# Kernel optimization log

Measured on AMD Instinct MI355X. Metric: run time of the kernel, lower is better.

The kernel has to match this reference:

```python
import jax, jax.numpy as jnp
import numpy as np

B, N, F_IN, H, MH, STEPS = 8192, 9, 15, 128, 256, 4
E_PER = 16
MASK_IDX = jnp.arange(8)  # mask = [True]*8 + [False]


def setup_inputs() -> dict:
    key = jax.random.key(0)
    ks = jax.random.split(key, 24)
    s = 0.05
    inp = {
        "obs": jax.random.normal(ks[0], (B, 135), jnp.float32),
        "edges": jax.random.randint(ks[1], (B, 2, E_PER), 0, N, jnp.int32),
        "enc_W": jax.random.normal(ks[2], (F_IN, H), jnp.float32) * s,
        "enc_b": jax.random.normal(ks[3], (H,), jnp.float32) * s,
        "msg_W1": jax.random.normal(ks[4], (STEPS, 2 * H, MH), jnp.float32) * s,
        "msg_b1": jax.random.normal(ks[5], (STEPS, MH), jnp.float32) * s,
        "msg_W2": jax.random.normal(ks[6], (STEPS, MH, MH), jnp.float32) * s,
        "msg_b2": jax.random.normal(ks[7], (STEPS, MH), jnp.float32) * s,
        "msg_W3": jax.random.normal(ks[8], (STEPS, MH, H), jnp.float32) * s,
        "msg_b3": jax.random.normal(ks[9], (STEPS, H), jnp.float32) * s,
        "gru_Wi": jax.random.normal(ks[10], (STEPS, H, 3 * H), jnp.float32) * s,
        "gru_Wh": jax.random.normal(ks[11], (STEPS, H, 3 * H), jnp.float32) * s,
        "gru_bi": jax.random.normal(ks[12], (STEPS, 3 * H), jnp.float32) * s,
        "gru_bh": jax.random.normal(ks[13], (STEPS, 3 * H), jnp.float32) * s,
        "dec_W1": jax.random.normal(ks[14], (H, MH), jnp.float32) * s,
        "dec_b1": jax.random.normal(ks[15], (MH,), jnp.float32) * s,
        "dec_W2": jax.random.normal(ks[16], (MH, MH), jnp.float32) * s,
        "dec_b2": jax.random.normal(ks[17], (MH,), jnp.float32) * s,
        "dec_W3": jax.random.normal(ks[18], (MH, 1), jnp.float32) * s,
        "dec_b3": jax.random.normal(ks[19], (1,), jnp.float32) * s,
    }
    return inp


def reference(obs, edges, enc_W, enc_b, msg_W1, msg_b1, msg_W2, msg_b2,
              msg_W3, msg_b3, gru_Wi, gru_Wh, gru_bi, gru_bh,
              dec_W1, dec_b1, dec_W2, dec_b2, dec_W3, dec_b3):
    BN = B * N
    x = obs.reshape(BN, F_IN)                       # [B*N, 15]
    x = jnp.tanh(x @ enc_W + enc_b)                 # encoder -> [B*N, H]

    # flatten per-graph edges into a global edge list, then add self-loops
    offsets = (jnp.arange(B, dtype=jnp.int32) * N)[:, None, None]
    eg = edges + offsets                            # [B, 2, 16]
    loops = jnp.arange(BN, dtype=jnp.int32)
    src = jnp.concatenate([eg[:, 0, :].reshape(-1), loops])  # x_j (source)
    dst = jnp.concatenate([eg[:, 1, :].reshape(-1), loops])  # x_i (target)
    deg = jax.ops.segment_sum(jnp.ones_like(dst, dtype=x.dtype), dst,
                              num_segments=BN)      # >=1 due to self-loops

    for s in range(STEPS):
        m = jnp.concatenate([x[dst], x[src]], axis=-1)       # [E, 2H]
        m = jnp.tanh(m @ msg_W1[s] + msg_b1[s])
        m = jnp.tanh(m @ msg_W2[s] + msg_b2[s])
        m = m @ msg_W3[s] + msg_b3[s]                        # [E, H]
        aggr = jax.ops.segment_sum(m, dst, num_segments=BN) / deg[:, None]
        # GRUCell(input=aggr, hidden=x), PyTorch gate order (r, z, n)
        gi = aggr @ gru_Wi[s] + gru_bi[s]
        gh = x @ gru_Wh[s] + gru_bh[s]
        ir, iz, inn = jnp.split(gi, 3, axis=-1)
        hr, hz, hn = jnp.split(gh, 3, axis=-1)
        r = jax.nn.sigmoid(ir + hr)
        z = jax.nn.sigmoid(iz + hz)
        n = jnp.tanh(inn + r * hn)
        x = (1.0 - z) * n + z * x

    d = jnp.tanh(x @ dec_W1 + dec_b1)
    d = jnp.tanh(d @ dec_W2 + dec_b2)
    d = d @ dec_W3 + dec_b3                                  # [B*N, 1]
    out = d.reshape(B, N)
    return out[:, MASK_IDX]                                  # [B, 8]
```

## Files before the change

### kernel.cpp

```cpp
#include <hip/hip_runtime.h>
#include <hip/hip_bf16.h>
#include <math.h>

#define BGR   8192
#define NND   9
#define BN    73728
#define NE    131072
#define ETOT  204800
#define H     128
#define MH    256
#define FIN   15

typedef __bf16 bf16_t;
typedef bf16_t bf16x8 __attribute__((ext_vector_type(8)));
typedef float  f32x4  __attribute__((ext_vector_type(4)));

__device__ __forceinline__ unsigned short f2bf(float f) {
    unsigned int u = __float_as_uint(f);
    u += 0x7fff + ((u >> 16) & 1);
    return (unsigned short)(u >> 16);
}
__device__ __forceinline__ unsigned int pkbf(float a, float b) {
    union { __hip_bfloat162 h; unsigned int u; } un;
    un.h = __float22bfloat162_rn(make_float2(a, b));
    return un.u;
}
__device__ __forceinline__ bf16x8 as_frag(int4 v) {
    union { int4 i; bf16x8 f; } u; u.i = v; return u.f;
}
__device__ __forceinline__ float fast_tanh(float v) {
    float e = __expf(2.0f * v);
    return 1.0f - __fdividef(2.0f, e + 1.0f);
}
__device__ __forceinline__ int sw_off(int m, int k) {
    return m * 256 + ((((k >> 3) ^ (m & 7)) << 3) | (k & 7));
}

__global__ void deg_kernel(const int* __restrict__ edges, float* __restrict__ inv_deg) {
    int g = blockIdx.x * 256 + threadIdx.x;
    if (g >= BGR) return;
    int cnt[NND];
#pragma unroll
    for (int n = 0; n < NND; ++n) cnt[n] = 1;
    for (int j = 0; j < 16; ++j) {
        int d = edges[g * 32 + 16 + j];
#pragma unroll
        for (int n = 0; n < NND; ++n) cnt[n] += (d == n) ? 1 : 0;
    }
#pragma unroll
    for (int n = 0; n < NND; ++n) inv_deg[g * NND + n] = 1.0f / (float)cnt[n];
}

__global__ void enc_kernel(const float* __restrict__ obs, const float* __restrict__ W,
                           const float* __restrict__ b, float* __restrict__ x) {
    int tid = blockIdx.x * 256 + threadIdx.x;
    int i = tid >> 7, h = tid & 127;
    float acc = b[h];
#pragma unroll
    for (int k = 0; k < FIN; ++k) acc += obs[i * FIN + k] * W[k * H + h];
    x[i * H + h] = tanhf(acc);
}

__global__ void wt_kernel(const float* __restrict__ W1, const float* __restrict__ W2,
                          const float* __restrict__ W3, const float* __restrict__ Wi,
                          const float* __restrict__ Wh, const float* __restrict__ dW1,
                          const float* __restrict__ dW2, unsigned short* __restrict__ out) {
    int idx = blockIdx.x * 256 + threadIdx.x;
    float v;
    if (idx < 262144) {
        int s = idx >> 16, r = idx & 65535, n = r >> 8, k = r & 255;
        v = W1[(s << 16) + (k << 8) + n];
    } else if (idx < 524288) {
        int i2 = idx - 262144;
        int s = i2 >> 16, r = i2 & 65535, n = r >> 8, k = r & 255;
        v = W2[(s << 16) + (k << 8) + n];
    } else if (idx < 655360) {
        int i3 = idx - 524288;
        int s = i3 >> 15, r = i3 & 32767, n = r >> 8, k = r & 255;
        v = W3[(s << 15) + (k << 7) + n];
    } else if (idx < 1179648) {
        int i4 = idx - 655360;
        int s = i4 >> 17, rr = i4 & 131071;
        int p = rr >> 8, k = rr & 255;
        int w = p >> 6, rem = p & 63;
        int gate = rem >> 4, c = rem & 15;
        int h = w * 16 + c;
        const int sb = s * 49152;
        if (gate == 0)      v = (k < 128) ? Wi[sb + k * 384 + h]       : Wh[sb + (k - 128) * 384 + h];
        else if (gate == 1) v = (k < 128) ? Wi[sb + k * 384 + 128 + h] : Wh[sb + (k - 128) * 384 + 128 + h];
        else if (gate == 2) v = (k < 128) ? Wi[sb + k * 384 + 256 + h] : 0.f;
        else                v = (k < 128) ? 0.f                        : Wh[sb + (k - 128) * 384 + 256 + h];
    } else if (idx < 1212416) {
        int i5 = idx - 1179648;
        int n = i5 >> 7, k = i5 & 127;
        v = dW1[k * 256 + n];
    } else {
        int i6 = idx - 1212416;
        int n = i6 >> 8, k = i6 & 255;
        v = dW2[k * 256 + n];
    }
    out[idx] = f2bf(v);
}

__global__ __launch_bounds__(512, 4) void msg_mfma(
        const float* __restrict__ x, const int* __restrict__ edges,
        const unsigned short* __restrict__ W1T, const float* __restrict__ b1,
        const unsigned short* __restrict__ W2T, const float* __restrict__ b2,
        const unsigned short* __restrict__ W3T,
        float* __restrict__ aggr) {
    __shared__ unsigned short buf[64 * 256];
    __shared__ int sdst[64];
    const int t  = threadIdx.x;
    const int e0 = blockIdx.x * 64;
    const int wv = t >> 6;
    const int ln = t & 63;
    const int lrow = ln & 15;
    const int lq   = ln >> 4;

    if (t < 64) {
        const int eg = e0 + t;
        sdst[t] = (eg < NE) ? ((eg >> 4) * NND + edges[(eg >> 4) * 32 + 16 + (eg & 15)])
                            : (eg - NE);
    }
    {
        const int row  = t >> 2;
        const int q    = t & 3;
        const int e    = row & 63;
        const int side = row >> 6;
        const int eg   = e0 + e;
        int node;
        if (eg < NE) {
            int g = eg >> 4, j = eg & 15;
            node = g * NND + (side ? edges[g * 32 + j] : edges[g * 32 + 16 + j]);
        } else {
            node = eg - NE;
        }
        const float* xs = x + (size_t)node * H + q * 32;
        const int kbase = side * 128 + q * 32;
#pragma unroll
        for (int i = 0; i < 8; ++i) {
            float4 v = *(const float4*)(xs + i * 4);
            uint2 o;
            o.x = pkbf(v.x, v.y); o.y = pkbf(v.z, v.w);
            *(uint2*)(buf + sw_off(e, kbase + i * 4)) = o;
        }
    }
    __syncthreads();

    const f32x4 zero = {0.f, 0.f, 0.f, 0.f};
    const int nbase = wv * 32;

    {
        f32x4 acc[4][2];
#pragma unroll
        for (int i = 0; i < 4; ++i)
#pragma unroll
            for (int j = 0; j < 2; ++j) acc[i][j] = zero;
        for (int kq = 0; kq < 8; ++kq) {
            const int ko = kq * 32 + lq * 8;
            bf16x8 af[4], bfr[2];
#pragma unroll
            for (int tm = 0; tm < 4; ++tm)
                af[tm] = as_frag(*(const int4*)(buf + sw_off(tm * 16 + lrow, ko)));
#pragma unroll
            for (int tn = 0; tn < 2; ++tn)
                bfr[tn] = as_frag(*(const int4*)(W1T + (size_t)(nbase + tn * 16 + lrow) * 256 + ko));
#pragma unroll
            for (int tm = 0; tm < 4; ++tm)
#pragma unroll
                for (int tn = 0; tn < 2; ++tn)
                    acc[tm][tn] = __builtin_amdgcn_mfma_f32_16x16x32_bf16(af[tm], bfr[tn], acc[tm][tn], 0, 0, 0);
        }
        __syncthreads();
#pragma unroll
        for (int tn = 0; tn < 2; ++tn) {
            const int n = nbase + tn * 16 + lrow;
            const float bias = b1[n];
#pragma unroll
            for (int tm = 0; tm < 4; ++tm)
#pragma unroll
                for (int r = 0; r < 4; ++r) {
                    const int m = tm * 16 + lq * 4 + r;
                    buf[sw_off(m, n)] = f2bf(fast_tanh(acc[tm][tn][r] + bias));
                }
        }
    }
    __syncthreads();

    {
        f32x4 acc[4][2];
#pragma unroll
        for (int i = 0; i < 4; ++i)
#pragma unroll
            for (int j = 0; j < 2; ++j) acc[i][j] = zero;
        for (int kq = 0; kq < 8; ++kq) {
            const int ko = kq * 32 + lq * 8;
            bf16x8 af[4], bfr[2];
#pragma unroll
            for (int tm = 0; tm < 4; ++tm)
                af[tm] = as_frag(*(const int4*)(buf + sw_off(tm * 16 + lrow, ko)));
#pragma unroll
            for (int tn = 0; tn < 2; ++tn)
                bfr[tn] = as_frag(*(const int4*)(W2T + (size_t)(nbase + tn * 16 + lrow) * 256 + ko));
#pragma unroll
            for (int tm = 0; tm < 4; ++tm)
#pragma unroll
                for (int tn = 0; tn < 2; ++tn)
                    acc[tm][tn] = __builtin_amdgcn_mfma_f32_16x16x32_bf16(af[tm], bfr[tn], acc[tm][tn], 0, 0, 0);
        }
        __syncthreads();
#pragma unroll
        for (int tn = 0; tn < 2; ++tn) {
            const int n = nbase + tn * 16 + lrow;
            const float bias = b2[n];
#pragma unroll
            for (int tm = 0; tm < 4; ++tm)
#pragma unroll
                for (int r = 0; r < 4; ++r) {
                    const int m = tm * 16 + lq * 4 + r;
                    buf[sw_off(m, n)] = f2bf(fast_tanh(acc[tm][tn][r] + bias));
                }
        }
    }
    __syncthreads();

    {
        const int n = wv * 16 + lrow;
        f32x4 acc3[4];
#pragma unroll
        for (int i = 0; i < 4; ++i) acc3[i] = zero;
        for (int kq = 0; kq < 8; ++kq) {
            const int ko = kq * 32 + lq * 8;
            bf16x8 af[4];
#pragma unroll
            for (int tm = 0; tm < 4; ++tm)
                af[tm] = as_frag(*(const int4*)(buf + sw_off(tm * 16 + lrow, ko)));
            const bf16x8 bfr = as_frag(*(const int4*)(W3T + (size_t)n * 256 + ko));
#pragma unroll
            for (int tm = 0; tm < 4; ++tm)
                acc3[tm] = __builtin_amdgcn_mfma_f32_16x16x32_bf16(af[tm], bfr, acc3[tm], 0, 0, 0);
        }
#pragma unroll
        for (int tm = 0; tm < 4; ++tm)
#pragma unroll
            for (int r = 0; r < 4; ++r) {
                const int m = tm * 16 + lq * 4 + r;
                atomicAdd(aggr + (size_t)sdst[m] * H + n, acc3[tm][r]);
            }
    }
}

__global__ __launch_bounds__(512, 4) void gru_mfma(
        float* __restrict__ x, float* __restrict__ aggr, const float* __restrict__ inv_deg,
        const unsigned short* __restrict__ WG, const float* __restrict__ b3m,
        const float* __restrict__ bi, const float* __restrict__ bh) {
    __shared__ unsigned short bufA[64 * 256];
    const int t = threadIdx.x;
    const int n0 = blockIdx.x * 64;
    const int wv = t >> 6, ln = t & 63, lrow = ln & 15, lq = ln >> 4;

    {
        const int m = t >> 3;
        const int q = t & 7;
        const int k0 = q * 32;
        const int node = n0 + m;
        if (q < 4) {
            const float scale = inv_deg[node];
            const float* src = aggr + (size_t)node * H + k0;
#pragma unroll
            for (int i = 0; i < 8; ++i) {
                float4 v = *(const float4*)(src + i * 4);
                const float4 bb = *(const float4*)(b3m + k0 + i * 4);
                v.x = v.x * scale + bb.x; v.y = v.y * scale + bb.y;
                v.z = v.z * scale + bb.z; v.w = v.w * scale + bb.w;
                uint2 o; o.x = pkbf(v.x, v.y); o.y = pkbf(v.z, v.w);
                *(uint2*)(bufA + sw_off(m, k0 + i * 4)) = o;
            }
        } else {
            const float* src = x + (size_t)node * H + (k0 - 128);
#pragma unroll
            for (int i = 0; i < 8; ++i) {
                float4 v = *(const float4*)(src + i * 4);
                uint2 o; o.x = pkbf(v.x, v.y); o.y = pkbf(v.z, v.w);
                *(uint2*)(bufA + sw_off(m, k0 + i * 4)) = o;
            }
        }
    }
    __syncthreads();

    const f32x4 zero = {0.f, 0.f, 0.f, 0.f};
    f32x4 acc[4][4];
#pragma unroll
    for (int i = 0; i < 4; ++i)
#pragma unroll
        for (int j = 0; j < 4; ++j) acc[i][j] = zero;

    for (int kq = 0; kq < 8; ++kq) {
        const int ko = kq * 32 + lq * 8;
        bf16x8 af[4], bfr[4];
#pragma unroll
        for (int tm = 0; tm < 4; ++tm)
            af[tm] = as_frag(*(const int4*)(bufA + sw_off(tm * 16 + lrow, ko)));
#pragma unroll
        for (int g = 0; g < 4; ++g)
            bfr[g] = as_frag(*(const int4*)(WG + (size_t)(wv * 64 + g * 16 + lrow) * 256 + ko));
#pragma unroll
        for (int tm = 0; tm < 4; ++tm)
#pragma unroll
            for (int g = 0; g < 4; ++g)
                acc[tm][g] = __builtin_amdgcn_mfma_f32_16x16x32_bf16(af[tm], bfr[g], acc[tm][g], 0, 0, 0);
    }

    {
        const int h = wv * 16 + lrow;
        const float b_r = bi[h] + bh[h];
        const float b_z = bi[128 + h] + bh[128 + h];
        const float b_n = bi[256 + h];
        const float b_h = bh[256 + h];
#pragma unroll
        for (int tm = 0; tm < 4; ++tm) {
#pragma unroll
            for (int r = 0; r < 4; ++r) {
                const int node = n0 + tm * 16 + lq * 4 + r;
                const float irhr = acc[tm][0][r] + b_r;
                const float izhz = acc[tm][1][r] + b_z;
                const float inn  = acc[tm][2][r] + b_n;
                const float hn   = acc[tm][3][r] + b_h;
                const float rg = 1.f / (1.f + expf(-irhr));
                const float zg = 1.f / (1.f + expf(-izhz));
                const float ng = tanhf(inn + rg * hn);
                const float xo = x[(size_t)node * H + h];
                x[(size_t)node * H + h] = (1.f - zg) * ng + zg * xo;
                aggr[(size_t)node * H + h] = 0.f;
            }
        }
    }
}

__global__ __launch_bounds__(256, 4) void dec_mfma(
        const float* __restrict__ x,
        const unsigned short* __restrict__ W1T, const float* __restrict__ b1,
        const unsigned short* __restrict__ W2T, const float* __restrict__ b2,
        const float* __restrict__ W3, const float* __restrict__ b3,
        float* __restrict__ out) {
    __shared__ unsigned short buf[64 * 256];
    const int t = threadIdx.x;
    const int id0 = blockIdx.x * 64;
    const int wv = t >> 6, ln = t & 63, lrow = ln & 15, lq = ln >> 4;
    const int nbase = wv * 64;

    {
        const int m = t >> 2, q = t & 3;
        const int id = id0 + m;
        const int node = (id >> 3) * NND + (id & 7);
        const float* src = x + (size_t)node * H + q * 32;
#pragma unroll
        for (int i = 0; i < 8; ++i) {
            float4 v = *(const float4*)(src + i * 4);
            uint2 o; o.x = pkbf(v.x, v.y); o.y = pkbf(v.z, v.w);
            *(uint2*)(buf + sw_off(m, q * 32 + i * 4)) = o;
        }
    }
    __syncthreads();

    const f32x4 zero = {0.f, 0.f, 0.f, 0.f};

    {
        f32x4 acc[4][4];
#pragma unroll
        for (int i = 0; i < 4; ++i)
#pragma unroll
            for (int j = 0; j < 4; ++j) acc[i][j] = zero;
        for (int kq = 0; kq < 4; ++kq) {
            const int ko = kq * 32 + lq * 8;
            bf16x8 af[4], bfr[4];
#pragma unroll
            for (int tm = 0; tm < 4; ++tm)
                af[tm] = as_frag(*(const int4*)(buf + sw_off(tm * 16 + lrow, ko)));
#pragma unroll
            for (int tn = 0; tn < 4; ++tn)
                bfr[tn] = as_frag(*(const int4*)(W1T + (size_t)(nbase + tn * 16 + lrow) * 128 + ko));
#pragma unroll
            for (int tm = 0; tm < 4; ++tm)
#pragma unroll
                for (int tn = 0; tn < 4; ++tn)
                    acc[tm][tn] = __builtin_amdgcn_mfma_f32_16x16x32_bf16(af[tm], bfr[tn], acc[tm][tn], 0, 0, 0);
        }
        __syncthreads();
#pragma unroll
        for (int tn = 0; tn < 4; ++tn) {
            const int n = nbase + tn * 16 + lrow;
            const float bias = b1[n];
#pragma unroll
            for (int tm = 0; tm < 4; ++tm)
#pragma unroll
                for (int r = 0; r < 4; ++r) {
                    const int m = tm * 16 + lq * 4 + r;
                    buf[sw_off(m, n)] = f2bf(fast_tanh(acc[tm][tn][r] + bias));
                }
        }
    }
    __syncthreads();

    {
        f32x4 acc[4][4];
#pragma unroll
        for (int i = 0; i < 4; ++i)
#pragma unroll
            for (int j = 0; j < 4; ++j) acc[i][j] = zero;
        for (int kq = 0; kq < 8; ++kq) {
            const int ko = kq * 32 + lq * 8;
            bf16x8 af[4], bfr[4];
#pragma unroll
            for (int tm = 0; tm < 4; ++tm)
                af[tm] = as_frag(*(const int4*)(buf + sw_off(tm * 16 + lrow, ko)));
#pragma unroll
            for (int tn = 0; tn < 4; ++tn)
                bfr[tn] = as_frag(*(const int4*)(W2T + (size_t)(nbase + tn * 16 + lrow) * 256 + ko));
#pragma unroll
            for (int tm = 0; tm < 4; ++tm)
#pragma unroll
                for (int tn = 0; tn < 4; ++tn)
                    acc[tm][tn] = __builtin_amdgcn_mfma_f32_16x16x32_bf16(af[tm], bfr[tn], acc[tm][tn], 0, 0, 0);
        }
        __syncthreads();
#pragma unroll
        for (int tn = 0; tn < 4; ++tn) {
            const int n = nbase + tn * 16 + lrow;
            const float bias = b2[n];
#pragma unroll
            for (int tm = 0; tm < 4; ++tm)
#pragma unroll
                for (int r = 0; r < 4; ++r) {
                    const int m = tm * 16 + lq * 4 + r;
                    buf[sw_off(m, n)] = f2bf(fast_tanh(acc[tm][tn][r] + bias));
                }
        }
    }
    __syncthreads();

    {
        const int m = t >> 2, p = t & 3;
        float s = 0.f;
#pragma unroll
        for (int i = 0; i < 64; ++i) {
            const int k = p * 64 + i;
            const float a = __uint_as_float((unsigned int)buf[sw_off(m, k)] << 16);
            s += a * W3[k];
        }
        s += __shfl_xor(s, 1);
        s += __shfl_xor(s, 2);
        if (p == 0) out[id0 + m] = s + b3[0];
    }
}

extern "C" void kernel_launch(void* const* d_in, const int* in_sizes, int n_in,
                              void* d_out, int out_size, void* d_ws, size_t ws_size,
                              hipStream_t stream) {
    const float* obs    = (const float*)d_in[0];
    const int*   edges  = (const int*)  d_in[1];
    const float* enc_W  = (const float*)d_in[2];
    const float* enc_b  = (const float*)d_in[3];
    const float* msg_W1 = (const float*)d_in[4];
    const float* msg_b1 = (const float*)d_in[5];
    const float* msg_W2 = (const float*)d_in[6];
    const float* msg_b2 = (const float*)d_in[7];
    const float* msg_W3 = (const float*)d_in[8];
    const float* msg_b3 = (const float*)d_in[9];
    const float* gru_Wi = (const float*)d_in[10];
    const float* gru_Wh = (const float*)d_in[11];
    const float* gru_bi = (const float*)d_in[12];
    const float* gru_bh = (const float*)d_in[13];
    const float* dec_W1 = (const float*)d_in[14];
    const float* dec_b1 = (const float*)d_in[15];
    const float* dec_W2 = (const float*)d_in[16];
    const float* dec_b2 = (const float*)d_in[17];
    const float* dec_W3 = (const float*)d_in[18];
    const float* dec_b3 = (const float*)d_in[19];

    float* x       = (float*)d_ws;
    float* aggr    = x + (size_t)BN * H;
    float* inv_deg = aggr + (size_t)BN * H;
    unsigned short* wbf = (unsigned short*)(inv_deg + BN);

    hipMemsetAsync(aggr, 0, (size_t)BN * H * sizeof(float), stream);
    deg_kernel<<<(BGR + 255) / 256, 256, 0, stream>>>(edges, inv_deg);
    wt_kernel<<<1277952 / 256, 256, 0, stream>>>(msg_W1, msg_W2, msg_W3, gru_Wi, gru_Wh,
                                                 dec_W1, dec_W2, wbf);
    enc_kernel<<<BN * H / 256, 256, 0, stream>>>(obs, enc_W, enc_b, x);

    for (int s = 0; s < 4; ++s) {
        const unsigned short* W1T = wbf + (size_t)s * 65536;
        const unsigned short* W2T = wbf + 262144 + (size_t)s * 65536;
        const unsigned short* W3T = wbf + 524288 + (size_t)s * 32768;
        const unsigned short* WGs = wbf + 655360 + (size_t)s * 131072;
        msg_mfma<<<ETOT / 64, 512, 0, stream>>>(
            x, edges,
            W1T, msg_b1 + (size_t)s * 256,
            W2T, msg_b2 + (size_t)s * 256,
            W3T,
            aggr);
        gru_mfma<<<BN / 64, 512, 0, stream>>>(
            x, aggr, inv_deg, WGs, msg_b3 + (size_t)s * 128,
            gru_bi + (size_t)s * 384, gru_bh + (size_t)s * 384);
    }

    dec_mfma<<<BGR * 8 / 64, 256, 0, stream>>>(
        x, wbf + 1179648, dec_b1, wbf + 1212416, dec_b2, dec_W3, dec_b3, (float*)d_out);
}
```

Baseline: 1.416 ms.

## Switch message MLP to 32x32x16 MFMA with double-buffered LDS

Rewrites the per-edge message MLP kernel to use 32x32x16 bf16 MFMA tiles instead of 16x16x32, with a 16-way XOR swizzle and two LDS buffers that alternate between layers. Alternating buffers removes the extra barrier that separated the last MFMA read from the activation writeback in each layer. The larger tile raises the compute done per fragment load, but the second 32 KB buffer doubles LDS use per block and may lower occupancy. The GRU and decoder kernels also get their k-loops fully unrolled and a hoisted weight pointer.

```diff
diff --git a/kernel.cpp b/kernel.cpp
--- a/kernel.cpp
+++ b/kernel.cpp
@@ -14,6 +14,7 @@
 typedef __bf16 bf16_t;
 typedef bf16_t bf16x8 __attribute__((ext_vector_type(8)));
 typedef float  f32x4  __attribute__((ext_vector_type(4)));
+typedef float  f32x16 __attribute__((ext_vector_type(16)));
 
 __device__ __forceinline__ unsigned short f2bf(float f) {
     unsigned int u = __float_as_uint(f);
@@ -31,6 +32,9 @@
 __device__ __forceinline__ float fast_tanh(float v) {
     float e = __expf(2.0f * v);
     return 1.0f - __fdividef(2.0f, e + 1.0f);
+}
+__device__ __forceinline__ int sw16(int m, int k) {
+    return m * 256 + ((((k >> 3) ^ (m & 15)) << 3) | (k & 7));
 }
 __device__ __forceinline__ int sw_off(int m, int k) {
     return m * 256 + ((((k >> 3) ^ (m & 7)) << 3) | (k & 7));
@@ -108,14 +112,15 @@
         const unsigned short* __restrict__ W2T, const float* __restrict__ b2,
         const unsigned short* __restrict__ W3T,
         float* __restrict__ aggr) {
-    __shared__ unsigned short buf[64 * 256];
+    __shared__ unsigned short bufA[64 * 256];
+    __shared__ unsigned short bufB[64 * 256];
     __shared__ int sdst[64];
     const int t  = threadIdx.x;
     const int e0 = blockIdx.x * 64;
     const int wv = t >> 6;
     const int ln = t & 63;
-    const int lrow = ln & 15;
-    const int lq   = ln >> 4;
+    const int l31 = ln & 31;
+    const int lh  = ln >> 5;
 
     if (t < 64) {
         const int eg = e0 + t;
@@ -142,111 +147,80 @@
             float4 v = *(const float4*)(xs + i * 4);
             uint2 o;
             o.x = pkbf(v.x, v.y); o.y = pkbf(v.z, v.w);
-            *(uint2*)(buf + sw_off(e, kbase + i * 4)) = o;
-        }
-    }
-    __syncthreads();
-
-    const f32x4 zero = {0.f, 0.f, 0.f, 0.f};
-    const int nbase = wv * 32;
-
-    {
-        f32x4 acc[4][2];
-#pragma unroll
-        for (int i = 0; i < 4; ++i)
-#pragma unroll
-            for (int j = 0; j < 2; ++j) acc[i][j] = zero;
-        for (int kq = 0; kq < 8; ++kq) {
-            const int ko = kq * 32 + lq * 8;
-            bf16x8 af[4], bfr[2];
-#pragma unroll
-            for (int tm = 0; tm < 4; ++tm)
-                af[tm] = as_frag(*(const int4*)(buf + sw_off(tm * 16 + lrow, ko)));
-#pragma unroll
-            for (int tn = 0; tn < 2; ++tn)
-                bfr[tn] = as_frag(*(const int4*)(W1T + (size_t)(nbase + tn * 16 + lrow) * 256 + ko));
-#pragma unroll
-            for (int tm = 0; tm < 4; ++tm)
-#pragma unroll
-                for (int tn = 0; tn < 2; ++tn)
-                    acc[tm][tn] = __builtin_amdgcn_mfma_f32_16x16x32_bf16(af[tm], bfr[tn], acc[tm][tn], 0, 0, 0);
-        }
-        __syncthreads();
-#pragma unroll
-        for (int tn = 0; tn < 2; ++tn) {
-            const int n = nbase + tn * 16 + lrow;
-            const float bias = b1[n];
-#pragma unroll
-            for (int tm = 0; tm < 4; ++tm)
-#pragma unroll
-                for (int r = 0; r < 4; ++r) {
-                    const int m = tm * 16 + lq * 4 + r;
-                    buf[sw_off(m, n)] = f2bf(fast_tanh(acc[tm][tn][r] + bias));
-                }
-        }
-    }
-    __syncthreads();
-
-    {
-        f32x4 acc[4][2];
-#pragma unroll
-        for (int i = 0; i < 4; ++i)
-#pragma unroll
-            for (int j = 0; j < 2; ++j) acc[i][j] = zero;
-        for (int kq = 0; kq < 8; ++kq) {
-            const int ko = kq * 32 + lq * 8;
-            bf16x8 af[4], bfr[2];
-#pragma unroll
-            for (int tm = 0; tm < 4; ++tm)
-                af[tm] = as_frag(*(const int4*)(buf + sw_off(tm * 16 + lrow, ko)));
-#pragma unroll
-            for (int tn = 0; tn < 2; ++tn)
-                bfr[tn] = as_frag(*(const int4*)(W2T + (size_t)(nbase + tn * 16 + lrow) * 256 + ko));
-#pragma unroll
-            for (int tm = 0; tm < 4; ++tm)
-#pragma unroll
-                for (int tn = 0; tn < 2; ++tn)
-                    acc[tm][tn] = __builtin_amdgcn_mfma_f32_16x16x32_bf16(af[tm], bfr[tn], acc[tm][tn], 0, 0, 0);
-        }
-        __syncthreads();
-#pragma unroll
-        for (int tn = 0; tn < 2; ++tn) {
-            const int n = nbase + tn * 16 + lrow;
-            const float bias = b2[n];
-#pragma unroll
-            for (int tm = 0; tm < 4; ++tm)
-#pragma unroll
-                for (int r = 0; r < 4; ++r) {
-                    const int m = tm * 16 + lq * 4 + r;
-                    buf[sw_off(m, n)] = f2bf(fast_tanh(acc[tm][tn][r] + bias));
-                }
-        }
-    }
-    __syncthreads();
-
-    {
-        const int n = wv * 16 + lrow;
-        f32x4 acc3[4];
-#pragma unroll
-        for (int i = 0; i < 4; ++i) acc3[i] = zero;
-        for (int kq = 0; kq < 8; ++kq) {
-            const int ko = kq * 32 + lq * 8;
-            bf16x8 af[4];
-#pragma unroll
-            for (int tm = 0; tm < 4; ++tm)
-                af[tm] = as_frag(*(const int4*)(buf + sw_off(tm * 16 + lrow, ko)));
-            const bf16x8 bfr = as_frag(*(const int4*)(W3T + (size_t)n * 256 + ko));
-#pragma unroll
-            for (int tm = 0; tm < 4; ++tm)
-                acc3[tm] = __builtin_amdgcn_mfma_f32_16x16x32_bf16(af[tm], bfr, acc3[tm], 0, 0, 0);
-        }
-#pragma unroll
-        for (int tm = 0; tm < 4; ++tm)
-#pragma unroll
-            for (int r = 0; r < 4; ++r) {
-                const int m = tm * 16 + lq * 4 + r;
-                atomicAdd(aggr + (size_t)sdst[m] * H + n, acc3[tm][r]);
-            }
+            *(uint2*)(bufA + sw16(e, kbase + i * 4)) = o;
+        }
+    }
+    __syncthreads();
+
+    {
+        f32x16 acc0, acc1;
+#pragma unroll
+        for (int i = 0; i < 16; ++i) { acc0[i] = 0.f; acc1[i] = 0.f; }
+        const unsigned short* wp = W1T + (size_t)(wv * 32 + l31) * 256 + lh * 8;
+#pragma unroll
+        for (int ks = 0; ks < 16; ++ks) {
+            const int kk = ks * 16 + lh * 8;
+            bf16x8 a0 = as_frag(*(const int4*)(bufA + sw16(l31, kk)));
+            bf16x8 a1 = as_frag(*(const int4*)(bufA + sw16(32 + l31, kk)));
+            bf16x8 bw = as_frag(*(const int4*)(wp + ks * 16));
+            acc0 = __builtin_amdgcn_mfma_f32_32x32x16_bf16(a0, bw, acc0, 0, 0, 0);
+            acc1 = __builtin_amdgcn_mfma_f32_32x32x16_bf16(a1, bw, acc1, 0, 0, 0);
+        }
+        const int n = wv * 32 + l31;
+        const float bias = b1[n];
+#pragma unroll
+        for (int reg = 0; reg < 16; ++reg) {
+            const int mrow = (reg & 3) + ((reg >> 2) << 3) + (lh << 2);
+            bufB[sw16(mrow, n)]      = f2bf(fast_tanh(acc0[reg] + bias));
+            bufB[sw16(32 + mrow, n)] = f2bf(fast_tanh(acc1[reg] + bias));
+        }
+    }
+    __syncthreads();
+
+    {
+        f32x16 acc0, acc1;
+#pragma unroll
+        for (int i = 0; i < 16; ++i) { acc0[i] = 0.f; acc1[i] = 0.f; }
+        const unsigned short* wp = W2T + (size_t)(wv * 32 + l31) * 256 + lh * 8;
+#pragma unroll
+        for (int ks = 0; ks < 16; ++ks) {
+            const int kk = ks * 16 + lh * 8;
+            bf16x8 a0 = as_frag(*(const int4*)(bufB + sw16(l31, kk)));
+            bf16x8 a1 = as_frag(*(const int4*)(bufB + sw16(32 + l31, kk)));
+            bf16x8 bw = as_frag(*(const int4*)(wp + ks * 16));
+            acc0 = __builtin_amdgcn_mfma_f32_32x32x16_bf16(a0, bw, acc0, 0, 0, 0);
+            acc1 = __builtin_amdgcn_mfma_f32_32x32x16_bf16(a1, bw, acc1, 0, 0, 0);
+        }
+        const int n = wv * 32 + l31;
+        const float bias = b2[n];
+#pragma unroll
+        for (int reg = 0; reg < 16; ++reg) {
+            const int mrow = (reg & 3) + ((reg >> 2) << 3) + (lh << 2);
+            bufA[sw16(mrow, n)]      = f2bf(fast_tanh(acc0[reg] + bias));
+            bufA[sw16(32 + mrow, n)] = f2bf(fast_tanh(acc1[reg] + bias));
+        }
+    }
+    __syncthreads();
+
+    {
+        const int mt = wv & 1, nq = wv >> 1;
+        const int n = nq * 32 + l31;
+        f32x16 acc;
+#pragma unroll
+        for (int i = 0; i < 16; ++i) acc[i] = 0.f;
+        const unsigned short* wp = W3T + (size_t)n * 256 + lh * 8;
+#pragma unroll
+        for (int ks = 0; ks < 16; ++ks) {
+            const int kk = ks * 16 + lh * 8;
+            bf16x8 a = as_frag(*(const int4*)(bufA + sw16(mt * 32 + l31, kk)));
+            bf16x8 bw = as_frag(*(const int4*)(wp + ks * 16));
+            acc = __builtin_amdgcn_mfma_f32_32x32x16_bf16(a, bw, acc, 0, 0, 0);
+        }
+#pragma unroll
+        for (int reg = 0; reg < 16; ++reg) {
+            const int m = mt * 32 + (reg & 3) + ((reg >> 2) << 3) + (lh << 2);
+            atomicAdd(aggr + (size_t)sdst[m] * H + n, acc[reg]);
+        }
     }
 }
 
@@ -295,6 +269,8 @@
 #pragma unroll
         for (int j = 0; j < 4; ++j) acc[i][j] = zero;
 
+    const unsigned short* wgp = WG + (size_t)(wv * 64 + lrow) * 256;
+#pragma unroll
     for (int kq = 0; kq < 8; ++kq) {
         const int ko = kq * 32 + lq * 8;
         bf16x8 af[4], bfr[4];
@@ -303,7 +279,7 @@
             af[tm] = as_frag(*(const int4*)(bufA + sw_off(tm * 16 + lrow, ko)));
 #pragma unroll
         for (int g = 0; g < 4; ++g)
-            bfr[g] = as_frag(*(const int4*)(WG + (size_t)(wv * 64 + g * 16 + lrow) * 256 + ko));
+            bfr[g] = as_frag(*(const int4*)(wgp + (size_t)g * 16 * 256 + ko));
 #pragma unroll
         for (int tm = 0; tm < 4; ++tm)
 #pragma unroll
@@ -371,6 +347,7 @@
         for (int i = 0; i < 4; ++i)
 #pragma unroll
             for (int j = 0; j < 4; ++j) acc[i][j] = zero;
+#pragma unroll
         for (int kq = 0; kq < 4; ++kq) {
             const int ko = kq * 32 + lq * 8;
             bf16x8 af[4], bfr[4];
@@ -408,6 +385,7 @@
         for (int i = 0; i < 4; ++i)
 #pragma unroll
             for (int j = 0; j < 4; ++j) acc[i][j] = zero;
+#pragma unroll
         for (int kq = 0; kq < 8; ++kq) {
             const int ko = kq * 32 + lq * 8;
             bf16x8 af[4], bfr[4];
```

Measured after the change: 1.340 ms. 1.06x faster.
